# Kernel optimization log

Measured on AMD Instinct MI355X. Metric: run time of the kernel, lower is better.

## Reference

```python
import jax, jax.numpy as jnp
import numpy as np
import math

N_HEAD, D_HEAD, D_MODEL = 12, 64, 768
ATT_SPAN = 512            # max_position_embeddings // stride**block_index
SCALE_FACTOR = 3          # 1 + 2 (relative attention: content + c2p + p2c)
CLS_TOKENS = 1            # num_highway_cls_tokens + 1
INF = 1e6
LN_EPS = 1e-5
SCALE = 1.0 / (math.sqrt(D_HEAD) * math.sqrt(SCALE_FACTOR))


def setup_inputs() -> dict:
    key = jax.random.key(0)
    ks = jax.random.split(key, 10)
    B, S = 2, 2048
    lin = lambda k, shape: jax.random.normal(k, shape, dtype=jnp.float32) * 0.02
    return {
        "query": jax.random.normal(ks[0], (B, S, D_MODEL), dtype=jnp.float32),
        "attention_mask": jnp.ones((B, S), dtype=jnp.float32),
        "pos_key_embed": jax.random.normal(ks[1], (2 * ATT_SPAN, D_MODEL), dtype=jnp.float32),
        "pos_query_embed": jax.random.normal(ks[2], (2 * ATT_SPAN, D_MODEL), dtype=jnp.float32),
        "Wq": lin(ks[3], (N_HEAD * D_HEAD, D_MODEL)),
        "bq": jnp.zeros((N_HEAD * D_HEAD,), dtype=jnp.float32),
        "Wk": lin(ks[4], (N_HEAD * D_HEAD, D_MODEL)),
        "Wv": lin(ks[5], (D_MODEL, D_MODEL)),
        "bv": jnp.zeros((D_MODEL,), dtype=jnp.float32),
        "Wpq": lin(ks[6], (N_HEAD * D_HEAD, D_MODEL)),
        "bpq": jnp.zeros((N_HEAD * D_HEAD,), dtype=jnp.float32),
        "Wpk": lin(ks[7], (N_HEAD * D_HEAD, D_MODEL)),
        "r_w_bias": jax.random.normal(ks[8], (N_HEAD, D_HEAD), dtype=jnp.float32) * 0.02,
        "ln_gamma": jnp.ones((D_MODEL,), dtype=jnp.float32),
        "ln_beta": jnp.zeros((D_MODEL,), dtype=jnp.float32),
    }


def _forward(query, attention_mask, pos_key_embed, pos_query_embed,
             Wq, bq, Wk, Wv, bv, Wpq, bpq, Wpk, r_w_bias, ln_gamma, ln_beta):
    B, S, _ = query.shape
    # self-attention: key = value = query
    v = query @ Wv.T + bv                                             # v_head projection
    qh = (query @ Wq.T + bq).reshape(B, S, N_HEAD, D_HEAD)
    kh = (query @ Wk.T).reshape(B, S, N_HEAD, D_HEAD)
    vh = v.reshape(B, S, N_HEAD, D_MODEL // N_HEAD)
    qh = (qh + r_w_bias) * SCALE                                       # bias + scale fused into q

    content = jnp.einsum('bind,bjnd->bnij', qh, kh)                    # [B,n,S,S]

    # ---- disentangled relative-position bias (DeBERTa-style c2p + p2c) ----
    pos_k = (pos_key_embed @ Wpk.T).reshape(2 * ATT_SPAN, N_HEAD, D_HEAD).transpose(1, 0, 2)          # [n,2span,d]
    pos_q = (pos_query_embed @ Wpq.T + bpq).reshape(2 * ATT_SPAN, N_HEAD, D_HEAD).transpose(1, 0, 2)  # [n,2span,d]
    qbn = qh.transpose(0, 2, 1, 3)                                     # [B,n,S,d] (already scaled)
    kbn = kh.transpose(0, 2, 1, 3)
    rel = jnp.arange(S)[:, None] - jnp.arange(S)[None, :]              # [S,S] query - key

    # content -> position
    c2p = jnp.einsum('bnid,njd->bnij', qbn, pos_k)                     # [B,n,S,2span]
    c2p_idx = jnp.clip(rel + ATT_SPAN, 0, 2 * ATT_SPAN - 1)
    c2p_score = jnp.take_along_axis(c2p, c2p_idx[None, None], axis=-1) # [B,n,S,S]

    # position -> content
    p2c = jnp.einsum('bnjd,nid->bnji', kbn * (1.0 / math.sqrt(D_HEAD * SCALE_FACTOR)), pos_q)  # [B,n,S,2span]
    p2c_idx = jnp.clip(-rel + ATT_SPAN, 0, 2 * ATT_SPAN - 1)
    p2c_score = jnp.take_along_axis(p2c, p2c_idx[None, None], axis=-1).swapaxes(-1, -2)        # [B,n,S,S]

    bias = c2p_score + p2c_score
    # zero out bias on cls rows and cls columns (the padding/concat trick in the source)
    keep = (jnp.arange(S) >= CLS_TOKENS).astype(bias.dtype)
    bias = bias * (keep[:, None] * keep[None, :])

    score = content + bias
    score = score - INF * (1.0 - attention_mask[:, None, None, :])
    prob = jax.nn.softmax(score, axis=-1)                              # attention_dropout = 0.0

    attn_vec = jnp.einsum('bnij,bjnd->bind', prob, vh).reshape(B, S, D_MODEL)
    # fused residual + LayerNorm(attn_out)
    mu = attn_vec.mean(-1, keepdims=True)
    var = ((attn_vec - mu) ** 2).mean(-1, keepdims=True)
    ln = (attn_vec - mu) / jnp.sqrt(var + LN_EPS) * ln_gamma + ln_beta
    return query + ln


def reference(query, attention_mask, pos_key_embed, pos_query_embed,
              Wq, bq, Wk, Wv, bv, Wpq, bpq, Wpk, r_w_bias, ln_gamma, ln_beta):
    return _forward(query, attention_mask, pos_key_embed, pos_query_embed,
                    Wq, bq, Wk, Wv, bv, Wpq, bpq, Wpk, r_w_bias, ln_gamma, ln_beta)
```

## Files before the change

kernel.cpp:

```cpp
#include <hip/hip_runtime.h>
#include <math.h>

#define NB     2
#define SEQ    2048
#define NHEAD  12
#define DMODEL 768
#define SPAN2  1024
#define SCALEF 0.07216878364870323f

typedef unsigned short ushort;
typedef unsigned int   uint;
typedef __attribute__((ext_vector_type(8))) short  bh8;
typedef __attribute__((ext_vector_type(4))) float  f32x4;
typedef __attribute__((ext_vector_type(4))) unsigned short us4;

__device__ inline ushort f2bf(float x) {
    uint u = __builtin_bit_cast(uint, x);
    u += 0x7FFFu + ((u >> 16) & 1u);
    return (ushort)(u >> 16);
}
__device__ inline float b2f(ushort h) {
    uint u = ((uint)h) << 16;
    return __builtin_bit_cast(float, u);
}

__device__ __forceinline__ void gld16(const ushort* g, ushort* l) {
    __builtin_amdgcn_global_load_lds(
        (const __attribute__((address_space(1))) void*)g,
        (__attribute__((address_space(3))) void*)l, 16, 0, 0);
}

__device__ __forceinline__ bh8 ldsfrag(const ushort* tile, int row, int slot) {
    return *(const bh8*)((const char*)tile + row * 128 + (((slot ^ (row & 7)) << 4)));
}

struct CvtArgs {
    const float* src[8];
    ushort*      dst[8];
    int          n[8];
};

__global__ __launch_bounds__(256) void cvt_bf16(CvtArgs a)
{
    const int seg = blockIdx.y;
    const int i   = (blockIdx.x * 256 + threadIdx.x) * 8;
    if (i >= a.n[seg]) return;
    const float4* s = (const float4*)(a.src[seg] + i);
    const float4 x = s[0], y = s[1];
    bh8 o;
    o[0] = (short)f2bf(x.x); o[1] = (short)f2bf(x.y);
    o[2] = (short)f2bf(x.z); o[3] = (short)f2bf(x.w);
    o[4] = (short)f2bf(y.x); o[5] = (short)f2bf(y.y);
    o[6] = (short)f2bf(y.z); o[7] = (short)f2bf(y.w);
    *(bh8*)(a.dst[seg] + i) = o;
}

__global__ __launch_bounds__(256) void proj_qkv(
    const ushort* __restrict__ X,
    const ushort* __restrict__ Wq, const ushort* __restrict__ Wk,
    const ushort* __restrict__ Wv,
    const float* __restrict__ bq, const float* __restrict__ rwb,
    const float* __restrict__ bv,
    ushort* __restrict__ qh, ushort* __restrict__ kh, ushort* __restrict__ vht)
{
    __shared__ ushort Xs [64 * 64];
    __shared__ ushort Wqs[64 * 64];
    __shared__ ushort Wks[64 * 64];
    __shared__ ushort Wvs[64 * 64];
    const int r0 = blockIdx.x * 64;
    const int n  = blockIdx.y;
    const int c0 = n * 64;
    const int tid  = threadIdx.x;
    const int w    = tid >> 6;
    const int lane = tid & 63;
    const int lo   = lane & 15;
    const int hi8  = (lane >> 4) * 8;
    const int g4   = (lane >> 4) * 4;
    const int w16  = w * 16;
    const int r8   = lane >> 3;
    const int sl   = lane & 7;
    const int slotA = hi8 >> 3;

    f32x4 aq[4] = {}, ak[4] = {}, av[4] = {};
    for (int k0 = 0; k0 < DMODEL; k0 += 64) {
        #pragma unroll
        for (int i = 0; i < 2; ++i) {
            const int c = i * 4 + w;
            const int r = c * 8 + r8;
            const int s = sl ^ (r & 7);
            gld16(X  + (size_t)(r0 + r) * DMODEL + k0 + s * 8, Xs  + c * 512);
            gld16(Wq + (size_t)(c0 + r) * DMODEL + k0 + s * 8, Wqs + c * 512);
            gld16(Wk + (size_t)(c0 + r) * DMODEL + k0 + s * 8, Wks + c * 512);
            gld16(Wv + (size_t)(c0 + r) * DMODEL + k0 + s * 8, Wvs + c * 512);
        }
        __syncthreads();
        const bh8 a0 = ldsfrag(Xs, w16 + lo, slotA);
        const bh8 a1 = ldsfrag(Xs, w16 + lo, 4 + slotA);
        #pragma unroll
        for (int ct = 0; ct < 4; ++ct) {
            const int row = ct * 16 + lo;
            aq[ct] = __builtin_amdgcn_mfma_f32_16x16x32_bf16(a0, ldsfrag(Wqs, row, slotA),     aq[ct], 0, 0, 0);
            aq[ct] = __builtin_amdgcn_mfma_f32_16x16x32_bf16(a1, ldsfrag(Wqs, row, 4 + slotA), aq[ct], 0, 0, 0);
            ak[ct] = __builtin_amdgcn_mfma_f32_16x16x32_bf16(a0, ldsfrag(Wks, row, slotA),     ak[ct], 0, 0, 0);
            ak[ct] = __builtin_amdgcn_mfma_f32_16x16x32_bf16(a1, ldsfrag(Wks, row, 4 + slotA), ak[ct], 0, 0, 0);
            av[ct] = __builtin_amdgcn_mfma_f32_16x16x32_bf16(a0, ldsfrag(Wvs, row, slotA),     av[ct], 0, 0, 0);
            av[ct] = __builtin_amdgcn_mfma_f32_16x16x32_bf16(a1, ldsfrag(Wvs, row, 4 + slotA), av[ct], 0, 0, 0);
        }
        __syncthreads();
    }

    const int rbase = r0 + w16 + g4;
    const int bb  = rbase >> 11;
    const int rr0 = rbase & (SEQ - 1);
    #pragma unroll
    for (int ct = 0; ct < 4; ++ct) {
        const int d = ct * 16 + lo;
        const int c = c0 + d;
        const float bqv = bq[c] + rwb[c];
        const float bvv = bv[c];
        us4 o;
        #pragma unroll
        for (int reg = 0; reg < 4; ++reg) {
            const size_t rowi = ((size_t)bb * NHEAD + n) * SEQ + rr0 + reg;
            qh[rowi * 64 + d] = f2bf((aq[ct][reg] + bqv) * SCALEF);
            kh[rowi * 64 + d] = f2bf(ak[ct][reg]);
            o[reg] = f2bf(av[ct][reg] + bvv);
        }
        *(us4*)&vht[(((size_t)bb * NHEAD + n) * 64 + d) * SEQ + rr0] = o;
    }
}

__global__ __launch_bounds__(256) void proj_pos(
    const ushort* __restrict__ PKe, const ushort* __restrict__ PQe,
    const ushort* __restrict__ Wpk, const ushort* __restrict__ Wpq,
    const float* __restrict__ bpq,
    ushort* __restrict__ pkp, ushort* __restrict__ pqp)
{
    __shared__ ushort Xk [32 * 64];
    __shared__ ushort Xq [32 * 64];
    __shared__ ushort Wks[64 * 64];
    __shared__ ushort Wqs[64 * 64];
    const int r0 = blockIdx.x * 32;
    const int n  = blockIdx.y;
    const int c0 = n * 64;
    const int tid  = threadIdx.x;
    const int w    = tid >> 6;
    const int lane = tid & 63;
    const int lo   = lane & 15;
    const int hi8  = (lane >> 4) * 8;
    const int g4   = (lane >> 4) * 4;
    const int wr   = w & 1;
    const int wc   = w >> 1;
    const int r8   = lane >> 3;
    const int sl   = lane & 7;
    const int slotA = hi8 >> 3;

    f32x4 apk[2] = {}, apq[2] = {};
    for (int k0 = 0; k0 < DMODEL; k0 += 64) {
        {
            const int r = w * 8 + r8;
            const int s = sl ^ (r & 7);
            gld16(PKe + (size_t)(r0 + r) * DMODEL + k0 + s * 8, Xk + w * 512);
            gld16(PQe + (size_t)(r0 + r) * DMODEL + k0 + s * 8, Xq + w * 512);
        }
        #pragma unroll
        for (int i = 0; i < 2; ++i) {
            const int c = i * 4 + w;
            const int r = c * 8 + r8;
            const int s = sl ^ (r & 7);
            gld16(Wpk + (size_t)(c0 + r) * DMODEL + k0 + s * 8, Wks + c * 512);
            gld16(Wpq + (size_t)(c0 + r) * DMODEL + k0 + s * 8, Wqs + c * 512);
        }
        __syncthreads();
        const bh8 xk0 = ldsfrag(Xk, wr * 16 + lo, slotA);
        const bh8 xk1 = ldsfrag(Xk, wr * 16 + lo, 4 + slotA);
        const bh8 xq0 = ldsfrag(Xq, wr * 16 + lo, slotA);
        const bh8 xq1 = ldsfrag(Xq, wr * 16 + lo, 4 + slotA);
        #pragma unroll
        for (int ct = 0; ct < 2; ++ct) {
            const int row = wc * 32 + ct * 16 + lo;
            apk[ct] = __builtin_amdgcn_mfma_f32_16x16x32_bf16(xk0, ldsfrag(Wks, row, slotA),     apk[ct], 0, 0, 0);
            apk[ct] = __builtin_amdgcn_mfma_f32_16x16x32_bf16(xk1, ldsfrag(Wks, row, 4 + slotA), apk[ct], 0, 0, 0);
            apq[ct] = __builtin_amdgcn_mfma_f32_16x16x32_bf16(xq0, ldsfrag(Wqs, row, slotA),     apq[ct], 0, 0, 0);
            apq[ct] = __builtin_amdgcn_mfma_f32_16x16x32_bf16(xq1, ldsfrag(Wqs, row, 4 + slotA), apq[ct], 0, 0, 0);
        }
        __syncthreads();
    }

    const int rr0 = r0 + wr * 16 + g4;
    #pragma unroll
    for (int ct = 0; ct < 2; ++ct) {
        const int d = wc * 32 + ct * 16 + lo;
        const int c = c0 + d;
        const float badd = bpq[c];
        #pragma unroll
        for (int reg = 0; reg < 4; ++reg) {
            const size_t rowi = ((size_t)n * SPAN2 + rr0 + reg);
            pkp[rowi * 64 + d] = f2bf(apk[ct][reg]);
            pqp[rowi * 64 + d] = f2bf((apq[ct][reg] + badd) * SCALEF);
        }
    }
}

__global__ __launch_bounds__(256) void cd_vec(
    const ushort* __restrict__ qh, const ushort* __restrict__ kh,
    const ushort* __restrict__ posk, const ushort* __restrict__ posq,
    float* __restrict__ cdv)
{
    __shared__ float pr[4][64];
    const int bn = blockIdx.y;
    const int n  = bn % NHEAD;
    const int tid = threadIdx.x;
    if (tid < 64) {
        pr[0][tid] = b2f(posk[((size_t)n * SPAN2) * 64 + tid]);
        pr[1][tid] = b2f(posk[((size_t)n * SPAN2 + SPAN2 - 1) * 64 + tid]);
        pr[2][tid] = b2f(posq[((size_t)n * SPAN2) * 64 + tid]);
        pr[3][tid] = b2f(posq[((size_t)n * SPAN2 + SPAN2 - 1) * 64 + tid]);
    }
    __syncthreads();
    const int row = blockIdx.x * 32 + (tid >> 3);
    const int e0  = (tid & 7) * 8;
    const bh8 q8 = *(const bh8*)&qh[((size_t)bn * SEQ + row) * 64 + e0];
    const bh8 k8 = *(const bh8*)&kh[((size_t)bn * SEQ + row) * 64 + e0];
    float a0 = 0.f, a1 = 0.f, a2 = 0.f, a3 = 0.f;
    #pragma unroll
    for (int t = 0; t < 8; ++t) {
        const float qv = b2f((ushort)q8[t]);
        const float kv = b2f((ushort)k8[t]);
        a0 += qv * pr[0][e0 + t];
        a1 += qv * pr[1][e0 + t];
        a2 += kv * pr[2][e0 + t];
        a3 += kv * pr[3][e0 + t];
    }
    #pragma unroll
    for (int off = 1; off <= 4; off <<= 1) {
        a0 += __shfl_xor(a0, off);
        a1 += __shfl_xor(a1, off);
        a2 += __shfl_xor(a2, off);
        a3 += __shfl_xor(a3, off);
    }
    if ((tid & 7) == 0) {
        cdv[((size_t)0 * NB * NHEAD + bn) * SEQ + row] = a0;
        cdv[((size_t)1 * NB * NHEAD + bn) * SEQ + row] = a1;
        cdv[((size_t)2 * NB * NHEAD + bn) * SEQ + row] = a2;
        cdv[((size_t)3 * NB * NHEAD + bn) * SEQ + row] = a3;
    }
}

__global__ __launch_bounds__(256, 3) void attn_mfma11(
    const ushort* __restrict__ qh, const ushort* __restrict__ kh,
    const ushort* __restrict__ vht, const ushort* __restrict__ posk,
    const ushort* __restrict__ posq, const float* __restrict__ mask,
    const float* __restrict__ cdv, float* __restrict__ attn)
{
    __shared__ ushort POS[128 * 64];
    __shared__ ushort Kb [64 * 64];
    __shared__ ushort Vb [64 * 64];
    __shared__ ushort TB1[64 * 68];
    __shared__ ushort TB2[64 * 68];

    const int id   = blockIdx.x;
    const int xcd  = id & 7;
    const int slot = id >> 3;
    const int bn   = xcd * 3 + (slot >> 5);
    const int i0   = (slot & 31) * 64;
    const int b    = bn / NHEAD;
    const int n    = bn % NHEAD;

    const int tid  = threadIdx.x;
    const int w    = tid >> 6;
    const int lane = tid & 63;
    const int lo   = lane & 15;
    const int hi8  = (lane >> 4) * 8;
    const int g4   = (lane >> 4) * 4;
    const int w16  = w * 16;
    const int r8   = lane >> 3;
    const int sl   = lane & 7;
    const int slotA = hi8 >> 3;

    const ushort* qrow = qh + ((size_t)bn * SEQ + i0 + w16 + lo) * 64;
    const bh8 qa0 = *(const bh8*)&qrow[hi8];
    const bh8 qa1 = *(const bh8*)&qrow[32 + hi8];

    const ushort* khb = kh   + (size_t)bn * SEQ * 64;
    const ushort* vtb = vht  + (size_t)bn * 64 * SEQ;
    const ushort* pkh = posk + (size_t)n * SPAN2 * 64;
    const ushort* pqh = posq + (size_t)n * SPAN2 * 64;
    const float*  mrw = mask + (size_t)b * SEQ;

    float C0r[4], C1r[4];
    {
        const float* C0p = cdv + (size_t)bn * SEQ;
        const float* C1p = cdv + ((size_t)NB * NHEAD + bn) * SEQ;
        #pragma unroll
        for (int reg = 0; reg < 4; ++reg) {
            C0r[reg] = C0p[i0 + w16 + g4 + reg];
            C1r[reg] = C1p[i0 + w16 + g4 + reg];
        }
    }
    const float* D0p = cdv + ((size_t)2 * NB * NHEAD + bn) * SEQ;
    const float* D1p = cdv + ((size_t)3 * NB * NHEAD + bn) * SEQ;

    f32x4 accPV[4] = {};
    float mrow[4] = {-1e30f, -1e30f, -1e30f, -1e30f};
    float lrow[4] = {0.f, 0.f, 0.f, 0.f};

    for (int j0 = 0; j0 < SEQ; j0 += 64) {
        const int d0base = i0 - j0 + 449;
        const bool clamp0 = (d0base <= -126);
        const bool clamp1 = (d0base >= 1023);

        if (!clamp0 && !clamp1) {
        #pragma unroll
        for (int i = 0; i < 2; ++i) {
            const int c = i * 4 + w;
            const int r = c * 8 + r8;
            const int s = sl ^ (r & 7);
            gld16(khb + (size_t)(j0 + r) * 64 + s * 8, Kb + c * 512);
        }
        #pragma unroll
        for (int i = 0; i < 4; ++i) {
            const int c = i * 4 + w;
            const int r = c * 8 + r8;
            const int s = sl ^ (r & 7);
            int gr = d0base + r; gr = gr < 0 ? 0 : (gr > SPAN2 - 1 ? SPAN2 - 1 : gr);
            gld16(pkh + (size_t)gr * 64 + s * 8, POS + c * 512);
        }
        __syncthreads();

        const bh8 ka0 = ldsfrag(Kb, w16 + lo, slotA);
        const bh8 ka1 = ldsfrag(Kb, w16 + lo, 4 + slotA);
        f32x4 z1[5];
        #pragma unroll
        for (int q = 0; q < 5; ++q) {
            const int u1 = (w + q) * 16 + lo;
            const bh8 pk0 = ldsfrag(POS, u1, slotA);
            const bh8 pk1 = ldsfrag(POS, u1, 4 + slotA);
            f32x4 a = {};
            a = __builtin_amdgcn_mfma_f32_16x16x32_bf16(qa0, pk0, a, 0, 0, 0);
            z1[q] = __builtin_amdgcn_mfma_f32_16x16x32_bf16(qa1, pk1, a, 0, 0, 0);
        }
        __syncthreads();

        #pragma unroll
        for (int i = 0; i < 4; ++i) {
            const int c = i * 4 + w;
            const int r = c * 8 + r8;
            const int s = sl ^ (r & 7);
            int gr = d0base + r; gr = gr < 0 ? 0 : (gr > SPAN2 - 1 ? SPAN2 - 1 : gr);
            gld16(pqh + (size_t)gr * 64 + s * 8, POS + c * 512);
        }
        #pragma unroll
        for (int i = 0; i < 2; ++i) {
            const int c = i * 4 + w;
            const int r = c * 8 + r8;
            const int s = sl ^ (r & 7);
            gld16(vtb + (size_t)r * SEQ + j0 + s * 8, Vb + c * 512);
        }
        #pragma unroll
        for (int q = 0; q < 5; ++q)
            #pragma unroll
            for (int reg = 0; reg < 4; ++reg) {
                const int jl = g4 + reg - q * 16 - lo + 63;
                if (jl >= 0 && jl < 64) {
                    const int il = w16 + g4 + reg;
                    const float v = ((i0 + il) >= 1 && (j0 + jl) >= 1) ? z1[q][reg] : 0.f;
                    TB1[jl * 68 + il] = f2bf(v);
                }
            }
        f32x4 accS[4];
        #pragma unroll
        for (int ct = 0; ct < 4; ++ct) {
            const bh8 kb0 = ldsfrag(Kb, ct * 16 + lo, slotA);
            const bh8 kb1 = ldsfrag(Kb, ct * 16 + lo, 4 + slotA);
            f32x4 z = {};
            z = __builtin_amdgcn_mfma_f32_16x16x32_bf16(qa0, kb0, z, 0, 0, 0);
            accS[ct] = __builtin_amdgcn_mfma_f32_16x16x32_bf16(qa1, kb1, z, 0, 0, 0);
        }
        float madd[4];
        #pragma unroll
        for (int reg = 0; reg < 4; ++reg)
            madd[reg] = -1e6f * (1.f - mrw[j0 + w16 + g4 + reg]);
        __syncthreads();

        #pragma unroll
        for (int q = 0; q < 5; ++q) {
            const int u2 = (3 - w + q) * 16 + lo;
            const bh8 pq0 = ldsfrag(POS, u2, slotA);
            const bh8 pq1 = ldsfrag(POS, u2, 4 + slotA);
            f32x4 z = {};
            z = __builtin_amdgcn_mfma_f32_16x16x32_bf16(ka0, pq0, z, 0, 0, 0);
            z = __builtin_amdgcn_mfma_f32_16x16x32_bf16(ka1, pq1, z, 0, 0, 0);
            #pragma unroll
            for (int reg = 0; reg < 4; ++reg) {
                const int il = (3 + q) * 16 + lo + g4 + reg - 63;
                if (il >= 0 && il < 64) {
                    const int jl = w16 + g4 + reg;
                    const float v = ((i0 + il) >= 1 && (j0 + jl) >= 1) ? z[reg] : 0.f;
                    TB2[jl * 68 + il] = f2bf(v + madd[reg]);
                }
            }
        }
        __syncthreads();

        float sv[4][4];
        #pragma unroll
        for (int ct = 0; ct < 4; ++ct) {
            const int jl = ct * 16 + lo;
            const us4 t1 = *(const us4*)&TB1[jl * 68 + w16 + g4];
            const us4 t2 = *(const us4*)&TB2[jl * 68 + w16 + g4];
            #pragma unroll
            for (int reg = 0; reg < 4; ++reg)
                sv[reg][ct] = accS[ct][reg] + b2f(t1[reg]) + b2f(t2[reg]);
        }
        float corr[4];
        char* pbase = (char*)POS + w * 2048;
        #pragma unroll
        for (int reg = 0; reg < 4; ++reg) {
            float rmax = fmaxf(fmaxf(sv[reg][0], sv[reg][1]), fmaxf(sv[reg][2], sv[reg][3]));
            rmax = fmaxf(rmax, __shfl_xor(rmax, 1));
            rmax = fmaxf(rmax, __shfl_xor(rmax, 2));
            rmax = fmaxf(rmax, __shfl_xor(rmax, 4));
            rmax = fmaxf(rmax, __shfl_xor(rmax, 8));
            const float mnew = fmaxf(mrow[reg], rmax);
            const float cc   = __expf(mrow[reg] - mnew);
            float psum = 0.f;
            const int prow = g4 + reg;
            #pragma unroll
            for (int ct = 0; ct < 4; ++ct) {
                const float p = __expf(sv[reg][ct] - mnew);
                psum += p;
                *(ushort*)(pbase + prow * 128 + ((((ct * 16 + lo) * 2)) ^ ((prow & 7) * 16))) = f2bf(p);
            }
            psum += __shfl_xor(psum, 1);
            psum += __shfl_xor(psum, 2);
            psum += __shfl_xor(psum, 4);
            psum += __shfl_xor(psum, 8);
            lrow[reg] = lrow[reg] * cc + psum;
            mrow[reg] = mnew;
            corr[reg] = cc;
        }

        {
            const bh8 pa0 = *(const bh8*)(pbase + lo * 128 + ((slotA << 4) ^ ((lo & 7) * 16)));
            const bh8 pa1 = *(const bh8*)(pbase + lo * 128 + (((4 + slotA) << 4) ^ ((lo & 7) * 16)));
            #pragma unroll
            for (int dt = 0; dt < 4; ++dt) {
                const bh8 vb0 = ldsfrag(Vb, dt * 16 + lo, slotA);
                const bh8 vb1 = ldsfrag(Vb, dt * 16 + lo, 4 + slotA);
                f32x4 a = accPV[dt];
                #pragma unroll
                for (int reg = 0; reg < 4; ++reg) a[reg] *= corr[reg];
                a = __builtin_amdgcn_mfma_f32_16x16x32_bf16(pa0, vb0, a, 0, 0, 0);
                accPV[dt] = __builtin_amdgcn_mfma_f32_16x16x32_bf16(pa1, vb1, a, 0, 0, 0);
            }
        }
        __syncthreads();

        } else {
        const float* Dp = clamp0 ? D0p : D1p;
        float Dvv[4];
        #pragma unroll
        for (int ct = 0; ct < 4; ++ct)
            Dvv[ct] = Dp[j0 + ct * 16 + lo];
        float maskadd[4];
        #pragma unroll
        for (int ct = 0; ct < 4; ++ct)
            maskadd[ct] = -1e6f * (1.f - mrw[j0 + ct * 16 + lo]);

        #pragma unroll
        for (int i = 0; i < 2; ++i) {
            const int c = i * 4 + w;
            const int r = c * 8 + r8;
            const int s = sl ^ (r & 7);
            gld16(khb + (size_t)(j0 + r) * 64 + s * 8, Kb + c * 512);
            gld16(vtb + (size_t)r * SEQ + j0 + s * 8, Vb + c * 512);
        }
        __syncthreads();

        f32x4 accS[4];
        #pragma unroll
        for (int ct = 0; ct < 4; ++ct) {
            const bh8 kb0 = ldsfrag(Kb, ct * 16 + lo, slotA);
            const bh8 kb1 = ldsfrag(Kb, ct * 16 + lo, 4 + slotA);
            f32x4 z = {};
            z = __builtin_amdgcn_mfma_f32_16x16x32_bf16(qa0, kb0, z, 0, 0, 0);
            accS[ct] = __builtin_amdgcn_mfma_f32_16x16x32_bf16(qa1, kb1, z, 0, 0, 0);
        }

        float corr[4];
        char* pbase = (char*)POS + w * 2048;
        #pragma unroll
        for (int reg = 0; reg < 4; ++reg) {
            const int il = w16 + g4 + reg;
            const int gi = i0 + il;
            const float Cvv = clamp0 ? C0r[reg] : C1r[reg];
            float s[4], rmax = -1e30f;
            #pragma unroll
            for (int ct = 0; ct < 4; ++ct) {
                const int jl = ct * 16 + lo;
                float v = accS[ct][reg];
                if (gi >= 1 && (j0 + jl) >= 1)
                    v += Cvv + Dvv[ct];
                v += maskadd[ct];
                s[ct] = v;
                rmax = fmaxf(rmax, v);
            }
            rmax = fmaxf(rmax, __shfl_xor(rmax, 1));
            rmax = fmaxf(rmax, __shfl_xor(rmax, 2));
            rmax = fmaxf(rmax, __shfl_xor(rmax, 4));
            rmax = fmaxf(rmax, __shfl_xor(rmax, 8));
            const float mnew = fmaxf(mrow[reg], rmax);
            const float cc   = __expf(mrow[reg] - mnew);
            float psum = 0.f;
            const int prow = g4 + reg;
            #pragma unroll
            for (int ct = 0; ct < 4; ++ct) {
                const float p = __expf(s[ct] - mnew);
                psum += p;
                *(ushort*)(pbase + prow * 128 + ((((ct * 16 + lo) * 2)) ^ ((prow & 7) * 16))) = f2bf(p);
            }
            psum += __shfl_xor(psum, 1);
            psum += __shfl_xor(psum, 2);
            psum += __shfl_xor(psum, 4);
            psum += __shfl_xor(psum, 8);
            lrow[reg] = lrow[reg] * cc + psum;
            mrow[reg] = mnew;
            corr[reg] = cc;
        }

        {
            const bh8 pa0 = *(const bh8*)(pbase + lo * 128 + ((slotA << 4) ^ ((lo & 7) * 16)));
            const bh8 pa1 = *(const bh8*)(pbase + lo * 128 + (((4 + slotA) << 4) ^ ((lo & 7) * 16)));
            #pragma unroll
            for (int dt = 0; dt < 4; ++dt) {
                const bh8 vb0 = ldsfrag(Vb, dt * 16 + lo, slotA);
                const bh8 vb1 = ldsfrag(Vb, dt * 16 + lo, 4 + slotA);
                f32x4 a = accPV[dt];
                #pragma unroll
                for (int reg = 0; reg < 4; ++reg) a[reg] *= corr[reg];
                a = __builtin_amdgcn_mfma_f32_16x16x32_bf16(pa0, vb0, a, 0, 0, 0);
                accPV[dt] = __builtin_amdgcn_mfma_f32_16x16x32_bf16(pa1, vb1, a, 0, 0, 0);
            }
        }
        __syncthreads();
        }
    }

    #pragma unroll
    for (int reg = 0; reg < 4; ++reg) {
        const int i = i0 + w16 + g4 + reg;
        const float inv = 1.f / lrow[reg];
        #pragma unroll
        for (int dt = 0; dt < 4; ++dt)
            attn[((size_t)b * SEQ + i) * DMODEL + n * 64 + dt * 16 + lo] =
                accPV[dt][reg] * inv;
    }
}

__global__ __launch_bounds__(256) void resid_ln(
    float* __restrict__ attn, const float* __restrict__ query,
    const float* __restrict__ gamma, const float* __restrict__ beta)
{
    const int b = blockIdx.y;
    const int i = blockIdx.x;
    const size_t base = ((size_t)b * SEQ + i) * DMODEL;
    const int tid = threadIdx.x;

    float x[3];
    #pragma unroll
    for (int s = 0; s < 3; ++s) x[s] = attn[base + s * 256 + tid];

    float sum = x[0] + x[1] + x[2];
    float sq  = x[0]*x[0] + x[1]*x[1] + x[2]*x[2];
    #pragma unroll
    for (int off = 32; off; off >>= 1) {
        sum += __shfl_xor(sum, off);
        sq  += __shfl_xor(sq, off);
    }
    __shared__ float red[2][4];
    const int w = tid >> 6;
    if ((tid & 63) == 0) { red[0][w] = sum; red[1][w] = sq; }
    __syncthreads();
    sum = red[0][0] + red[0][1] + red[0][2] + red[0][3];
    sq  = red[1][0] + red[1][1] + red[1][2] + red[1][3];

    const float mu  = sum * (1.f / DMODEL);
    const float var = sq * (1.f / DMODEL) - mu * mu;
    const float inv = rsqrtf(var + 1e-5f);

    #pragma unroll
    for (int s = 0; s < 3; ++s) {
        const int c = s * 256 + tid;
        attn[base + c] = query[base + c] + (x[s] - mu) * inv * gamma[c] + beta[c];
    }
}

extern "C" void kernel_launch(void* const* d_in, const int* in_sizes, int n_in,
                              void* d_out, int out_size, void* d_ws, size_t ws_size,
                              hipStream_t stream)
{
    const float* query = (const float*)d_in[0];
    const float* mask  = (const float*)d_in[1];
    const float* pke   = (const float*)d_in[2];
    const float* pqe   = (const float*)d_in[3];
    const float* Wq    = (const float*)d_in[4];
    const float* bq    = (const float*)d_in[5];
    const float* Wk    = (const float*)d_in[6];
    const float* Wv    = (const float*)d_in[7];
    const float* bv    = (const float*)d_in[8];
    const float* Wpq   = (const float*)d_in[9];
    const float* bpq   = (const float*)d_in[10];
    const float* Wpk   = (const float*)d_in[11];
    const float* rwb   = (const float*)d_in[12];
    const float* gamma = (const float*)d_in[13];
    const float* beta  = (const float*)d_in[14];

    float* out = (float*)d_out;

    const int Q_N  = NB * SEQ * DMODEL;
    const int P_N  = SPAN2 * DMODEL;
    const int W_N  = DMODEL * DMODEL;
    const size_t QKV_ELEMS = (size_t)NB * NHEAD * SEQ * 64;
    const size_t POS_ELEMS = (size_t)NHEAD * SPAN2 * 64;

    ushort* xb   = (ushort*)d_ws;
    ushort* pkeb = xb   + Q_N;
    ushort* pqeb = pkeb + P_N;
    ushort* wqb  = pqeb + P_N;
    ushort* wkb  = wqb  + W_N;
    ushort* wvb  = wkb  + W_N;
    ushort* wpqb = wvb  + W_N;
    ushort* wpkb = wpqb + W_N;
    ushort* qh   = wpkb + W_N;
    ushort* kh   = qh   + QKV_ELEMS;
    ushort* vht  = kh   + QKV_ELEMS;
    ushort* pkp  = vht  + QKV_ELEMS;
    ushort* pqp  = pkp  + POS_ELEMS;
    float*  cdv  = (float*)(pqp + POS_ELEMS);

    dim3 blk(256);

    CvtArgs ca;
    ca.src[0] = query; ca.dst[0] = xb;   ca.n[0] = Q_N;
    ca.src[1] = pke;   ca.dst[1] = pkeb; ca.n[1] = P_N;
    ca.src[2] = pqe;   ca.dst[2] = pqeb; ca.n[2] = P_N;
    ca.src[3] = Wq;    ca.dst[3] = wqb;  ca.n[3] = W_N;
    ca.src[4] = Wk;    ca.dst[4] = wkb;  ca.n[4] = W_N;
    ca.src[5] = Wv;    ca.dst[5] = wvb;  ca.n[5] = W_N;
    ca.src[6] = Wpq;   ca.dst[6] = wpqb; ca.n[6] = W_N;
    ca.src[7] = Wpk;   ca.dst[7] = wpkb; ca.n[7] = W_N;
    cvt_bf16<<<dim3((Q_N / 8 + 255) / 256, 8), blk, 0, stream>>>(ca);

    proj_qkv<<<dim3(NB * SEQ / 64, NHEAD), blk, 0, stream>>>(
        xb, wqb, wkb, wvb, bq, rwb, bv, qh, kh, vht);
    proj_pos<<<dim3(SPAN2 / 32, NHEAD), blk, 0, stream>>>(
        pkeb, pqeb, wpkb, wpqb, bpq, pkp, pqp);

    cd_vec<<<dim3(SEQ / 32, NB * NHEAD), blk, 0, stream>>>(
        qh, kh, pkp, pqp, cdv);

    attn_mfma11<<<dim3(NB * NHEAD * (SEQ / 64)), blk, 0, stream>>>(
        qh, kh, vht, pkp, pqp, mask, cdv, out);

    resid_ln<<<dim3(SEQ, NB), blk, 0, stream>>>(out, query, gamma, beta);
}
```

Baseline: 211.6 us.

## Load pos-query fragments directly to registers and drop two block barriers per tile

```diff
diff --git a/kernel.cpp b/kernel.cpp
--- a/kernel.cpp
+++ b/kernel.cpp
@@ -247,7 +247,7 @@
     }
 }
 
-__global__ __launch_bounds__(256, 3) void attn_mfma11(
+__global__ __launch_bounds__(256, 3) void attn_mfma12(
     const ushort* __restrict__ qh, const ushort* __restrict__ kh,
     const ushort* __restrict__ vht, const ushort* __restrict__ posk,
     const ushort* __restrict__ posq, const float* __restrict__ mask,
@@ -317,6 +317,7 @@
             const int r = c * 8 + r8;
             const int s = sl ^ (r & 7);
             gld16(khb + (size_t)(j0 + r) * 64 + s * 8, Kb + c * 512);
+            gld16(vtb + (size_t)r * SEQ + j0 + s * 8, Vb + c * 512);
         }
         #pragma unroll
         for (int i = 0; i < 4; ++i) {
@@ -328,9 +329,20 @@
         }
         __syncthreads();
 
-        const bh8 ka0 = ldsfrag(Kb, w16 + lo, slotA);
-        const bh8 ka1 = ldsfrag(Kb, w16 + lo, 4 + slotA);
-        f32x4 z1[5];
+        bh8 pq0r[5], pq1r[5];
+        #pragma unroll
+        for (int q = 0; q < 5; ++q) {
+            int r = d0base + (3 - w + q) * 16 + lo;
+            r = r < 0 ? 0 : (r > SPAN2 - 1 ? SPAN2 - 1 : r);
+            const ushort* pb = pqh + (size_t)r * 64;
+            pq0r[q] = *(const bh8*)&pb[hi8];
+            pq1r[q] = *(const bh8*)&pb[32 + hi8];
+        }
+        float madd[4];
+        #pragma unroll
+        for (int reg = 0; reg < 4; ++reg)
+            madd[reg] = -1e6f * (1.f - mrw[j0 + w16 + g4 + reg]);
+
         #pragma unroll
         for (int q = 0; q < 5; ++q) {
             const int u1 = (w + q) * 16 + lo;
@@ -338,36 +350,20 @@
             const bh8 pk1 = ldsfrag(POS, u1, 4 + slotA);
             f32x4 a = {};
             a = __builtin_amdgcn_mfma_f32_16x16x32_bf16(qa0, pk0, a, 0, 0, 0);
-            z1[q] = __builtin_amdgcn_mfma_f32_16x16x32_bf16(qa1, pk1, a, 0, 0, 0);
-        }
-        __syncthreads();
-
-        #pragma unroll
-        for (int i = 0; i < 4; ++i) {
-            const int c = i * 4 + w;
-            const int r = c * 8 + r8;
-            const int s = sl ^ (r & 7);
-            int gr = d0base + r; gr = gr < 0 ? 0 : (gr > SPAN2 - 1 ? SPAN2 - 1 : gr);
-            gld16(pqh + (size_t)gr * 64 + s * 8, POS + c * 512);
-        }
-        #pragma unroll
-        for (int i = 0; i < 2; ++i) {
-            const int c = i * 4 + w;
-            const int r = c * 8 + r8;
-            const int s = sl ^ (r & 7);
-            gld16(vtb + (size_t)r * SEQ + j0 + s * 8, Vb + c * 512);
-        }
-        #pragma unroll
-        for (int q = 0; q < 5; ++q)
+            a = __builtin_amdgcn_mfma_f32_16x16x32_bf16(qa1, pk1, a, 0, 0, 0);
             #pragma unroll
             for (int reg = 0; reg < 4; ++reg) {
                 const int jl = g4 + reg - q * 16 - lo + 63;
                 if (jl >= 0 && jl < 64) {
                     const int il = w16 + g4 + reg;
-                    const float v = ((i0 + il) >= 1 && (j0 + jl) >= 1) ? z1[q][reg] : 0.f;
+                    const float v = ((i0 + il) >= 1 && (j0 + jl) >= 1) ? a[reg] : 0.f;
                     TB1[jl * 68 + il] = f2bf(v);
                 }
             }
+        }
+
+        const bh8 ka0 = ldsfrag(Kb, w16 + lo, slotA);
+        const bh8 ka1 = ldsfrag(Kb, w16 + lo, 4 + slotA);
         f32x4 accS[4];
         #pragma unroll
         for (int ct = 0; ct < 4; ++ct) {
@@ -377,20 +373,12 @@
             z = __builtin_amdgcn_mfma_f32_16x16x32_bf16(qa0, kb0, z, 0, 0, 0);
             accS[ct] = __builtin_amdgcn_mfma_f32_16x16x32_bf16(qa1, kb1, z, 0, 0, 0);
         }
-        float madd[4];
-        #pragma unroll
-        for (int reg = 0; reg < 4; ++reg)
-            madd[reg] = -1e6f * (1.f - mrw[j0 + w16 + g4 + reg]);
-        __syncthreads();
 
         #pragma unroll
         for (int q = 0; q < 5; ++q) {
-            const int u2 = (3 - w + q) * 16 + lo;
-            const bh8 pq0 = ldsfrag(POS, u2, slotA);
-            const bh8 pq1 = ldsfrag(POS, u2, 4 + slotA);
             f32x4 z = {};
-            z = __builtin_amdgcn_mfma_f32_16x16x32_bf16(ka0, pq0, z, 0, 0, 0);
-            z = __builtin_amdgcn_mfma_f32_16x16x32_bf16(ka1, pq1, z, 0, 0, 0);
+            z = __builtin_amdgcn_mfma_f32_16x16x32_bf16(ka0, pq0r[q], z, 0, 0, 0);
+            z = __builtin_amdgcn_mfma_f32_16x16x32_bf16(ka1, pq1r[q], z, 0, 0, 0);
             #pragma unroll
             for (int reg = 0; reg < 4; ++reg) {
                 const int il = (3 + q) * 16 + lo + g4 + reg - 63;
@@ -660,7 +648,7 @@
     cd_vec<<<dim3(SEQ / 32, NB * NHEAD), blk, 0, stream>>>(
         qh, kh, pkp, pqp, cdv);
 
-    attn_mfma11<<<dim3(NB * NHEAD * (SEQ / 64)), blk, 0, stream>>>(
+    attn_mfma12<<<dim3(NB * NHEAD * (SEQ / 64)), blk, 0, stream>>>(
         qh, kh, vht, pkp, pqp, mask, cdv, out);
 
     resid_ln<<<dim3(SEQ, NB), blk, 0, stream>>>(out, query, gamma, beta);
```

Measured after the change: 317.7 us. 50.2% more time.
